# Kernel optimization log

Hardware: AMD Instinct MI355X
Metric: run time of the kernel (lower is better)

Reference implementation:

```python
import jax, jax.numpy as jnp
import numpy as np
from math import sqrt

NUM_HEAD = 16
HEAD_DIM = 64  # out_dim // num_head = 1024 // 16


def setup_inputs() -> dict:
    key = jax.random.key(0)
    ks = jax.random.split(key, 6)
    B, L, D = 2, 2048, 1024
    s = 1.0 / sqrt(D)
    return {
        "x": jax.random.normal(ks[0], (B, L, D), jnp.float32),
        "position_embedding": jax.random.normal(ks[1], (1, NUM_HEAD, L, L), jnp.float32),
        "Wq": jax.random.normal(ks[2], (D, D), jnp.float32) * s,
        "Wk": jax.random.normal(ks[3], (D, D), jnp.float32) * s,
        "Wv": jax.random.normal(ks[4], (D, D), jnp.float32) * s,
        "Wo": jax.random.normal(ks[5], (D, D), jnp.float32) * s,
    }


def reference(x, position_embedding, Wq, Wk, Wv, Wo):
    # x: [B, L, D]; torch Linear(y = x @ W.T) -> here weights stored as [in, out]
    B, L, D = x.shape
    H, Hd = NUM_HEAD, HEAD_DIM
    q = (x @ Wq).reshape(B, L, H, Hd).transpose(0, 2, 1, 3)  # [B,H,L,Hd]
    k = (x @ Wk).reshape(B, L, H, Hd).transpose(0, 2, 1, 3)
    v = (x @ Wv).reshape(B, L, H, Hd).transpose(0, 2, 1, 3)
    scores = jnp.einsum("bhqd,bhkd->bhqk", q, k) / sqrt(Hd)  # [B,H,L,L]
    scores = scores + position_embedding
    attn = jax.nn.softmax(scores, axis=-1)
    out = jnp.einsum("bhqk,bhkd->bhqd", attn, v)  # [B,H,L,Hd]
    out = out.transpose(0, 2, 1, 3).reshape(B, L, H * Hd)
    return out @ Wo
```

## Files before the change

kernel.cpp:

```cpp
#include <hip/hip_runtime.h>
#include <hip/hip_bf16.h>
#include <stdint.h>

typedef __hip_bfloat16 bf16;
typedef __attribute__((ext_vector_type(8))) short bf16x8;
typedef __attribute__((ext_vector_type(4))) float f32x4;
typedef __attribute__((ext_vector_type(16))) float f32x16;
typedef __attribute__((ext_vector_type(4))) unsigned u32x4;

#define B_  2
#define L_  2048
#define D_  1024
#define H_  16
#define HD_ 64
#define BH_ 32
#define L2E 1.4426950408889634f
#define HSZ ((size_t)BH_ * L_ * HD_)

#define DEV static __device__ __forceinline__

DEV short f2bf(float f) {
    bf16 h = __float2bfloat16(f);
    return __builtin_bit_cast(short, h);
}

DEV unsigned pk2(float lo, float hi) {
    unsigned a = (unsigned short)__builtin_bit_cast(unsigned short, __float2bfloat16(lo));
    unsigned b = (unsigned short)__builtin_bit_cast(unsigned short, __float2bfloat16(hi));
    return a | (b << 16);
}

DEV f32x4 mfma16(bf16x8 a, bf16x8 b, f32x4 c) {
    return __builtin_amdgcn_mfma_f32_16x16x32_bf16(a, b, c, 0, 0, 0);
}
DEV f32x16 mfma32(bf16x8 a, bf16x8 b, f32x16 c) {
    return __builtin_amdgcn_mfma_f32_32x32x16_bf16(a, b, c, 0, 0, 0);
}

DEV void async_ld16(const void* g, void* lds_uniform) {
    __builtin_amdgcn_global_load_lds((const __attribute__((address_space(1))) void*)g,
                                     (__attribute__((address_space(3))) void*)lds_uniform,
                                     16, 0, 0);
}

DEV int swz(int row, int col) {
    int blk = (row << 3) + (col >> 3);
    blk ^= (row & 7);
    return (blk << 3) + (col & 7);
}

__global__ __launch_bounds__(256) void k_cast_x(const float* __restrict__ x,
                                                bf16* __restrict__ xb, int n8) {
    int i = blockIdx.x * 256 + threadIdx.x;
    if (i >= n8) return;
    const float4* src = (const float4*)x + (size_t)i * 2;
    float4 a = src[0], b = src[1];
    bf16x8 v;
    v[0]=f2bf(a.x); v[1]=f2bf(a.y); v[2]=f2bf(a.z); v[3]=f2bf(a.w);
    v[4]=f2bf(b.x); v[5]=f2bf(b.y); v[6]=f2bf(b.z); v[7]=f2bf(b.w);
    *(bf16x8*)(xb + (size_t)i * 8) = v;
}

__global__ __launch_bounds__(256) void k_cast_wT(const float* __restrict__ W0, const float* __restrict__ W1,
                                                 const float* __restrict__ W2, const float* __restrict__ W3,
                                                 bf16* __restrict__ WT) {
    const float* W = (blockIdx.z == 0) ? W0 : (blockIdx.z == 1) ? W1 : (blockIdx.z == 2) ? W2 : W3;
    __shared__ float tile[64][65];
    const int r0 = blockIdx.y * 64, c0 = blockIdx.x * 64;
    const int tx = threadIdx.x & 63, ty = threadIdx.x >> 6;
    #pragma unroll
    for (int i = 0; i < 16; ++i) {
        int r = ty + i * 4;
        tile[r][tx] = W[(size_t)(r0 + r) * D_ + c0 + tx];
    }
    __syncthreads();
    bf16* out = WT + (size_t)blockIdx.z * D_ * D_;
    #pragma unroll
    for (int i = 0; i < 16; ++i) {
        int n = ty + i * 4;
        out[(size_t)(c0 + n) * D_ + r0 + tx] = __float2bfloat16(tile[tx][n]);
    }
}

template <int MODE, int TM>
__global__ __launch_bounds__(256) void k_gemm(const bf16* __restrict__ A, const bf16* __restrict__ BT,
                                              void* __restrict__ C) {
    constexpr int MI = TM / 32;
    __shared__ __align__(16) bf16 As[TM * 64];
    __shared__ __align__(16) bf16 Bs[128 * 64];
    const int t = threadIdx.x;
    const int w = t >> 6, lane = t & 63;
    const int lr = lane & 15, lg = lane >> 4;
    const int wr = (w >> 1) * (TM / 2), wc = (w & 1) * 64;
    const size_t am0 = (size_t)blockIdx.y * TM;
    const size_t bn0 = (size_t)blockIdx.x * 128;

    f32x4 acc[MI][4] = {};

    for (int kt = 0; kt < 1024 / 64; ++kt) {
        const int k0 = kt * 64;
        if (kt) __syncthreads();
        #pragma unroll
        for (int c = 0; c < TM / 32; ++c) {
            int phys = c * 256 + t;
            int lb = phys ^ ((phys >> 3) & 7);
            int row = lb >> 3, cb = lb & 7;
            int ldsoff = (c * 256 + w * 64) * 8;
            async_ld16(A + (am0 + row) * 1024 + k0 + cb * 8, (void*)(As + ldsoff));
        }
        #pragma unroll
        for (int c = 0; c < 4; ++c) {
            int phys = c * 256 + t;
            int lb = phys ^ ((phys >> 3) & 7);
            int row = lb >> 3, cb = lb & 7;
            int ldsoff = (c * 256 + w * 64) * 8;
            async_ld16(BT + (bn0 + row) * 1024 + k0 + cb * 8, (void*)(Bs + ldsoff));
        }
        __syncthreads();
        bf16x8 af[MI][2], bfv[4][2];
        #pragma unroll
        for (int mi = 0; mi < MI; ++mi)
            #pragma unroll
            for (int ks = 0; ks < 2; ++ks)
                af[mi][ks] = *(const bf16x8*)(As + swz(wr + mi * 16 + lr, ks * 32 + lg * 8));
        #pragma unroll
        for (int ni = 0; ni < 4; ++ni)
            #pragma unroll
            for (int ks = 0; ks < 2; ++ks)
                bfv[ni][ks] = *(const bf16x8*)(Bs + swz(wc + ni * 16 + lr, ks * 32 + lg * 8));
        #pragma unroll
        for (int mi = 0; mi < MI; ++mi)
            #pragma unroll
            for (int ni = 0; ni < 4; ++ni) {
                acc[mi][ni] = mfma16(af[mi][0], bfv[ni][0], acc[mi][ni]);
                acc[mi][ni] = mfma16(af[mi][1], bfv[ni][1], acc[mi][ni]);
            }
    }

    #pragma unroll
    for (int mi = 0; mi < MI; ++mi)
        #pragma unroll
        for (int ni = 0; ni < 4; ++ni) {
            const size_t gm0 = am0 + wr + mi * 16 + lg * 4;
            const size_t gn  = bn0 + wc + ni * 16 + lr;
            float v0 = acc[mi][ni][0], v1 = acc[mi][ni][1];
            float v2 = acc[mi][ni][2], v3 = acc[mi][ni][3];
            if (MODE == 1) {
                float* dst = (float*)C + gm0 * 1024 + gn;
                dst[0] = v0; dst[1024] = v1; dst[2048] = v2; dst[3072] = v3;
            } else {
                const int which = (int)(gn >> 10);
                const int hh = (int)((gn >> 6) & 15);
                const int d  = (int)(gn & 63);
                const int bbb = (int)(gm0 >> 11);
                const int ll  = (int)(gm0 & 2047);
                if (which == 2) {
                    bf16* vdst = (bf16*)C + 3 * HSZ + ((size_t)(bbb * H_ + hh) * HD_ + d) * L_ + ll;
                    uint2 pv;
                    pv.x = pk2(v0, v1);
                    pv.y = pk2(v2, v3);
                    *(uint2*)vdst = pv;
                } else {
                    float s = (which == 0) ? 0.18033688011112042f : 1.0f;
                    bf16* dst = (bf16*)C + (size_t)which * HSZ
                              + ((size_t)(bbb * H_ + hh) * L_ + ll) * HD_ + d;
                    dst[0]   = __float2bfloat16(v0 * s);
                    dst[64]  = __float2bfloat16(v1 * s);
                    dst[128] = __float2bfloat16(v2 * s);
                    dst[192] = __float2bfloat16(v3 * s);
                }
            }
        }
}

__global__ __launch_bounds__(256, 2) void k_attn(const bf16* __restrict__ Qb, const bf16* __restrict__ Kb,
                                                 const bf16* __restrict__ VTb, const float* __restrict__ PE,
                                                 bf16* __restrict__ Ob) {
    __shared__ __align__(16) char shm[73728];

    const int bid = blockIdx.x;
    const int sw  = (bid & 7) * 64 + (bid >> 3);
    const int qt  = sw & 31, h = sw >> 5;
    const int t   = threadIdx.x;
    const int w   = t >> 6, l = t & 63;
    const int qs  = w & 1, b = w >> 1;
    const int q0  = qt * 64 + qs * 32;
    const int lq  = l & 31;
    const int lh  = l >> 5;

    const int pb = (lq >> 2) & 3;
    const int prow = lq + (pb == 1 ? 4 : (pb == 2 ? -4 : 0));

    bf16x8 Qf[4];
    #pragma unroll
    for (int dm = 0; dm < 4; ++dm)
        Qf[dm] = *(const bf16x8*)(Qb + ((size_t)(b * H_ + h) * L_ + q0 + lq) * HD_ + dm * 16 + lh * 8);

    const bf16*  kb    = Kb  + (size_t)(b * H_ + h) * L_ * HD_;
    const bf16*  vbase = VTb + (size_t)h * HD_ * L_;
    const float* peq   = PE  + ((size_t)h * L_ + q0) * L_;

    const int k_srcoff  = (l >> 3) * HD_ + (((l & 7) ^ (l >> 3)) * 8);
    const int vlb = (l & 7) ^ (l >> 3);
    const size_t v_lane = (size_t)(vlb >> 2) * ((size_t)H_ * HD_ * L_)
                        + (size_t)(l >> 3) * L_ + (vlb & 3) * 8;
    const int pe_srcoff = (l >> 3) * L_ + (((l & 7) ^ (l >> 3)) * 4);

    int kro[4];
    #pragma unroll
    for (int dm = 0; dm < 4; ++dm)
        kro[dm] = prow * 64 + (((dm * 2 + lh) ^ (prow & 7)) * 8);
    int vro[2][2];
    #pragma unroll
    for (int d0 = 0; d0 < 2; ++d0)
        #pragma unroll
        for (int m = 0; m < 2; ++m)
            vro[d0][m] = (d0 * 32 + lq) * 64 + (((b * 4 + m * 2 + lh) ^ (lq & 7)) * 8);
    int peo[4];
    #pragma unroll
    for (int g = 0; g < 4; ++g)
        peo[g] = lq * 32 + ((((g >> 1) * 4 + (g & 1) + lh * 2) ^ (lq & 7)) * 4);

#define SH_K(BUF)  (shm + (BUF) * 24576 + b * 4096)
#define SH_V(BUF)  (shm + (BUF) * 24576 + 8192)
#define SH_PE(BUF) (shm + (BUF) * 24576 + 16384 + qs * 4096)

    f32x16 o[2] = {};
    float mrun = -3e38f, lpart = 0.f;

#define STAGE(BUF, TILE) {                                                              \
    const int kv0_ = (TILE) * 32;                                                       \
    _Pragma("unroll") for (int i = 0; i < 2; ++i) {                                     \
        const int c = 2 * qs + i;                                                       \
        async_ld16(kb + (size_t)(kv0_ + c * 8) * HD_ + k_srcoff, (void*)(SH_K(BUF) + c * 1024)); \
    }                                                                                   \
    _Pragma("unroll") for (int i = 0; i < 2; ++i) {                                     \
        const int cv = 2 * w + i;                                                       \
        async_ld16(vbase + v_lane + (size_t)(cv * 8) * L_ + kv0_, (void*)(SH_V(BUF) + cv * 1024)); \
    }                                                                                   \
    _Pragma("unroll") for (int i = 0; i < 2; ++i) {                                     \
        const int c = 2 * b + i;                                                        \
        async_ld16(peq + (size_t)(c * 8) * L_ + kv0_ + pe_srcoff, (void*)(SH_PE(BUF) + c * 1024)); \
    }                                                                                   \
}

#define COMPUTE(BUF) {                                                                  \
    const bf16*  KL = (const bf16*)SH_K(BUF);                                           \
    const bf16*  VL = (const bf16*)SH_V(BUF);                                           \
    const float* PL = (const float*)SH_PE(BUF);                                         \
    bf16x8 kf0_ = *(const bf16x8*)(KL + kro[0]);                                        \
    bf16x8 kf1_ = *(const bf16x8*)(KL + kro[1]);                                        \
    bf16x8 kf2_ = *(const bf16x8*)(KL + kro[2]);                                        \
    bf16x8 kf3_ = *(const bf16x8*)(KL + kro[3]);                                        \
    f32x16 s = {};                                                                      \
    s = mfma32(kf0_, Qf[0], s);                                                         \
    s = mfma32(kf1_, Qf[1], s);                                                         \
    s = mfma32(kf2_, Qf[2], s);                                                         \
    s = mfma32(kf3_, Qf[3], s);                                                         \
    float4 pef_[4];                                                                     \
    _Pragma("unroll") for (int g = 0; g < 4; ++g)                                       \
        pef_[g] = *(const float4*)(PL + peo[g]);                                        \
    float v_[16];                                                                       \
    _Pragma("unroll") for (int r = 0; r < 16; ++r)                                      \
        v_[r] = fmaf(pef_[r >> 2][r & 3], L2E, s[r]);                                   \
    float t0_ = fmaxf(fmaxf(v_[0], v_[1]), fmaxf(v_[2], v_[3]));                        \
    float t1_ = fmaxf(fmaxf(v_[4], v_[5]), fmaxf(v_[6], v_[7]));                        \
    float t2_ = fmaxf(fmaxf(v_[8], v_[9]), fmaxf(v_[10], v_[11]));                      \
    float t3_ = fmaxf(fmaxf(v_[12], v_[13]), fmaxf(v_[14], v_[15]));                    \
    float vmh_ = fmaxf(fmaxf(t0_, t1_), fmaxf(t2_, t3_));                               \
    float vm_ = fmaxf(vmh_, __shfl_xor(vmh_, 32, 64));                                  \
    float mold_ = mrun;                                                                 \
    float mnew_ = mold_;                                                                \
    if (!__all(vm_ <= mold_ + 10.f)) {                                                  \
        mnew_ = fmaxf(mold_, vm_);                                                      \
        float scl_ = __builtin_amdgcn_exp2f(mold_ - mnew_);                             \
        mrun = mnew_;                                                                   \
        lpart *= scl_;                                                                  \
        _Pragma("unroll") for (int r = 0; r < 16; ++r) { o[0][r] *= scl_; o[1][r] *= scl_; } \
    }                                                                                   \
    float p_[16], ssum_ = 0.f;                                                          \
    _Pragma("unroll") for (int r = 0; r < 16; ++r) {                                    \
        p_[r] = __builtin_amdgcn_exp2f(v_[r] - mnew_);                                  \
        ssum_ += p_[r];                                                                 \
    }                                                                                   \
    lpart += ssum_;                                                                     \
    unsigned a_[8];                                                                     \
    _Pragma("unroll") for (int j = 0; j < 8; ++j)                                       \
        a_[j] = pk2(p_[2 * j], p_[2 * j + 1]);                                          \
    u32x4 w0v_ = { a_[0], a_[1], a_[2], a_[3] };                                        \
    u32x4 w1v_ = { a_[4], a_[5], a_[6], a_[7] };                                        \
    bf16x8 pf0_ = __builtin_bit_cast(bf16x8, w0v_);                                     \
    bf16x8 pf1_ = __builtin_bit_cast(bf16x8, w1v_);                                     \
    o[0] = mfma32(*(const bf16x8*)(VL + vro[0][0]), pf0_, o[0]);                        \
    o[0] = mfma32(*(const bf16x8*)(VL + vro[0][1]), pf1_, o[0]);                        \
    o[1] = mfma32(*(const bf16x8*)(VL + vro[1][0]), pf0_, o[1]);                        \
    o[1] = mfma32(*(const bf16x8*)(VL + vro[1][1]), pf1_, o[1]);                        \
}

#define STEP(BUF, T, PFT) {                                                             \
    asm volatile("s_waitcnt vmcnt(12)" ::: "memory");                                   \
    __builtin_amdgcn_s_barrier();                                                       \
    COMPUTE(BUF)                                                                        \
    __builtin_amdgcn_s_barrier();                                                       \
    STAGE(BUF, PFT)                                                                     \
}

    STAGE(0, 0)
    STAGE(1, 1)
    STAGE(2, 2)

    for (int tp = 0; tp < 21; ++tp) {
        const int e = 3 * tp;
        const int f0 = (e + 3 < 64) ? e + 3 : 63;
        const int f1 = (e + 4 < 64) ? e + 4 : 63;
        const int f2 = (e + 5 < 64) ? e + 5 : 63;
        STEP(0, e,     f0)
        STEP(1, e + 1, f1)
        STEP(2, e + 2, f2)
    }
    asm volatile("s_waitcnt vmcnt(12)" ::: "memory");
    __builtin_amdgcn_s_barrier();
    COMPUTE(0)
#undef STEP
#undef COMPUTE
#undef STAGE
#undef SH_K
#undef SH_V
#undef SH_PE

    asm volatile("s_waitcnt vmcnt(0)" ::: "memory");

    float lsum = lpart + __shfl_xor(lpart, 32, 64);
    float inv = __builtin_amdgcn_rcpf(lsum);
    #pragma unroll
    for (int d0 = 0; d0 < 2; ++d0)
        #pragma unroll
        for (int r = 0; r < 16; r += 2) {
            float e0 = o[d0][r] * inv;
            float e1 = o[d0][r + 1] * inv;
            int d = d0 * 32 + ((r & 3) + 8 * (r >> 2)) + lh * 4;
            *(unsigned*)(Ob + ((size_t)b * L_ + q0 + lq) * D_ + h * HD_ + d) = pk2(e0, e1);
        }
}

extern "C" void kernel_launch(void* const* d_in, const int* in_sizes, int n_in,
                              void* d_out, int out_size, void* d_ws, size_t ws_size,
                              hipStream_t stream) {
    const float* x  = (const float*)d_in[0];
    const float* pe = (const float*)d_in[1];
    const float* Wq = (const float*)d_in[2];
    const float* Wk = (const float*)d_in[3];
    const float* Wv = (const float*)d_in[4];
    const float* Wo = (const float*)d_in[5];
    float* out = (float*)d_out;

    const size_t MD = (size_t)4096 * 1024;

    bf16* Xb  = (bf16*)d_ws;
    bf16* WT  = Xb + MD;
    bf16* Qb  = WT + MD;
    bf16* Kb  = Qb + HSZ;
    bf16* Vb  = Kb + HSZ;
    bf16* VTb = Vb + HSZ;
    bf16* Ob  = VTb + HSZ;

    k_cast_x<<<2048, 256, 0, stream>>>(x, Xb, 4096 * 1024 / 8);
    k_cast_wT<<<dim3(16, 16, 4), 256, 0, stream>>>(Wq, Wk, Wv, Wo, WT);
    k_gemm<0, 128><<<dim3(24, 32), 256, 0, stream>>>(Xb, WT, (void*)Qb);
    k_attn<<<512, 256, 0, stream>>>(Qb, Kb, VTb, pe, Ob);
    k_gemm<1, 64><<<dim3(8, 64), 256, 0, stream>>>(Ob, WT + (size_t)3072 * 1024, (void*)out);
}
```

Before: 160.1 us.

## Merge cast kernels and restructure attention pipeline to one barrier per step

```diff
diff --git a/kernel.cpp b/kernel.cpp
--- a/kernel.cpp
+++ b/kernel.cpp
@@ -49,24 +49,26 @@
     return (blk << 3) + (col & 7);
 }
 
-__global__ __launch_bounds__(256) void k_cast_x(const float* __restrict__ x,
-                                                bf16* __restrict__ xb, int n8) {
-    int i = blockIdx.x * 256 + threadIdx.x;
-    if (i >= n8) return;
-    const float4* src = (const float4*)x + (size_t)i * 2;
-    float4 a = src[0], b = src[1];
-    bf16x8 v;
-    v[0]=f2bf(a.x); v[1]=f2bf(a.y); v[2]=f2bf(a.z); v[3]=f2bf(a.w);
-    v[4]=f2bf(b.x); v[5]=f2bf(b.y); v[6]=f2bf(b.z); v[7]=f2bf(b.w);
-    *(bf16x8*)(xb + (size_t)i * 8) = v;
-}
-
-__global__ __launch_bounds__(256) void k_cast_wT(const float* __restrict__ W0, const float* __restrict__ W1,
-                                                 const float* __restrict__ W2, const float* __restrict__ W3,
-                                                 bf16* __restrict__ WT) {
-    const float* W = (blockIdx.z == 0) ? W0 : (blockIdx.z == 1) ? W1 : (blockIdx.z == 2) ? W2 : W3;
+__global__ __launch_bounds__(256) void k_prep(const float* __restrict__ x,
+                                              const float* __restrict__ W0, const float* __restrict__ W1,
+                                              const float* __restrict__ W2, const float* __restrict__ W3,
+                                              bf16* __restrict__ xb, bf16* __restrict__ WT) {
     __shared__ float tile[64][65];
-    const int r0 = blockIdx.y * 64, c0 = blockIdx.x * 64;
+    if (blockIdx.x < 2048) {
+        int i = blockIdx.x * 256 + threadIdx.x;
+        const float4* src = (const float4*)x + (size_t)i * 2;
+        float4 a = src[0], b = src[1];
+        bf16x8 v;
+        v[0]=f2bf(a.x); v[1]=f2bf(a.y); v[2]=f2bf(a.z); v[3]=f2bf(a.w);
+        v[4]=f2bf(b.x); v[5]=f2bf(b.y); v[6]=f2bf(b.z); v[7]=f2bf(b.w);
+        *(bf16x8*)(xb + (size_t)i * 8) = v;
+        return;
+    }
+    const int zz = blockIdx.x - 2048;
+    const int z = zz >> 8, rem = zz & 255;
+    const int by = rem >> 4, bx = rem & 15;
+    const float* W = (z == 0) ? W0 : (z == 1) ? W1 : (z == 2) ? W2 : W3;
+    const int r0 = by * 64, c0 = bx * 64;
     const int tx = threadIdx.x & 63, ty = threadIdx.x >> 6;
     #pragma unroll
     for (int i = 0; i < 16; ++i) {
@@ -74,7 +76,7 @@
         tile[r][tx] = W[(size_t)(r0 + r) * D_ + c0 + tx];
     }
     __syncthreads();
-    bf16* out = WT + (size_t)blockIdx.z * D_ * D_;
+    bf16* out = WT + (size_t)z * D_ * D_;
     #pragma unroll
     for (int i = 0; i < 16; ++i) {
         int n = ty + i * 4;
@@ -297,28 +299,26 @@
     o[1] = mfma32(*(const bf16x8*)(VL + vro[1][1]), pf1_, o[1]);                        \
 }
 
-#define STEP(BUF, T, PFT) {                                                             \
-    asm volatile("s_waitcnt vmcnt(12)" ::: "memory");                                   \
+#define STEP(BUF, SBUF, PFT) {                                                          \
+    asm volatile("s_waitcnt vmcnt(6)" ::: "memory");                                    \
     __builtin_amdgcn_s_barrier();                                                       \
+    STAGE(SBUF, PFT)                                                                    \
     COMPUTE(BUF)                                                                        \
-    __builtin_amdgcn_s_barrier();                                                       \
-    STAGE(BUF, PFT)                                                                     \
 }
 
     STAGE(0, 0)
     STAGE(1, 1)
-    STAGE(2, 2)
 
     for (int tp = 0; tp < 21; ++tp) {
         const int e = 3 * tp;
-        const int f0 = (e + 3 < 64) ? e + 3 : 63;
-        const int f1 = (e + 4 < 64) ? e + 4 : 63;
-        const int f2 = (e + 5 < 64) ? e + 5 : 63;
-        STEP(0, e,     f0)
-        STEP(1, e + 1, f1)
-        STEP(2, e + 2, f2)
-    }
-    asm volatile("s_waitcnt vmcnt(12)" ::: "memory");
+        const int f0 = (e + 2 < 64) ? e + 2 : 63;
+        const int f1 = (e + 3 < 64) ? e + 3 : 63;
+        const int f2 = (e + 4 < 64) ? e + 4 : 63;
+        STEP(0, 2, f0)
+        STEP(1, 0, f1)
+        STEP(2, 1, f2)
+    }
+    asm volatile("s_waitcnt vmcnt(6)" ::: "memory");
     __builtin_amdgcn_s_barrier();
     COMPUTE(0)
 #undef STEP
@@ -364,8 +364,7 @@
     bf16* VTb = Vb + HSZ;
     bf16* Ob  = VTb + HSZ;
 
-    k_cast_x<<<2048, 256, 0, stream>>>(x, Xb, 4096 * 1024 / 8);
-    k_cast_wT<<<dim3(16, 16, 4), 256, 0, stream>>>(Wq, Wk, Wv, Wo, WT);
+    k_prep<<<3072, 256, 0, stream>>>(x, Wq, Wk, Wv, Wo, Xb, WT);
     k_gemm<0, 128><<<dim3(24, 32), 256, 0, stream>>>(Xb, WT, (void*)Qb);
     k_attn<<<512, 256, 0, stream>>>(Qb, Kb, VTb, pe, Ob);
     k_gemm<1, 64><<<dim3(8, 64), 256, 0, stream>>>(Ob, WT + (size_t)3072 * 1024, (void*)out);
```

New measurement: 162.5 us. Within noise of the previous version (+1.5%).
